# Kernel optimization log

Measured on AMD Instinct MI355X. Metric: run time of the kernel, lower is better.

The kernel has to match this reference:

```python
import jax, jax.numpy as jnp
import numpy as np

N = 100000      # nodes
E = 1600000     # edges (avg degree 16)
D_IN = 256
D_OUT = 128

def setup_inputs() -> dict:
    key = jax.random.key(0)
    k1, k2, k3, k4, k5 = jax.random.split(key, 5)
    x = jax.random.normal(k1, (N, D_IN), dtype=jnp.float32)
    row = jax.random.randint(k2, (E,), 0, N)           # destination node of each edge (adj row index)
    col = jax.random.randint(k3, (E,), 0, N)           # source node (adj col index)
    vals = jnp.ones((E,), dtype=jnp.float32)           # adjacency values
    W = jax.random.normal(k4, (D_IN, D_OUT), dtype=jnp.float32) * (1.0 / np.sqrt(D_IN))
    b = jax.random.normal(k5, (D_OUT,), dtype=jnp.float32) * 0.01
    return {"x": x, "row": row, "col": col, "vals": vals, "W": W, "b": b}

def reference(x, row, col, vals, W, b):
    # support = Linear(x)
    support = x @ W + b                                   # [N, D_OUT]
    # symmetric normalization: D^-1/2 A D^-1/2 (degree = row sums of adj)
    deg = jax.ops.segment_sum(vals, row, num_segments=N)  # [N]
    d_inv_sqrt = jnp.where(deg > 0, jax.lax.rsqrt(jnp.maximum(deg, 1e-12)), 0.0)
    norm_vals = vals * d_inv_sqrt[row] * d_inv_sqrt[col]  # [E]
    # output = spmm(adj_norm, support): gather source features, scale, scatter-add to rows
    out = jax.ops.segment_sum(norm_vals[:, None] * support[col], row, num_segments=N)  # [N, D_OUT]
    return out
```

## Files before the change

kernel.cpp:

```cpp
#include <hip/hip_runtime.h>
#include <hip/hip_bf16.h>

#define DIN 256
#define DOUT 128

typedef float f32x4 __attribute__((ext_vector_type(4)));
typedef __bf16 bf16x8 __attribute__((ext_vector_type(8)));
typedef unsigned short u16x8 __attribute__((ext_vector_type(8)));

__device__ __forceinline__ unsigned short f2bf(float f) {
    __bf16 h = (__bf16)f;
    return *(unsigned short*)&h;
}

__global__ void gcn_wconv(const float* __restrict__ W, unsigned short* __restrict__ Wt) {
    int id = blockIdx.x * blockDim.x + threadIdx.x;
    int c = id >> 8;
    int k = id & 255;
    Wt[c * 256 + k] = f2bf(W[k * DOUT + c]);
}

__global__ __launch_bounds__(256) void gcn_gemm_count(
        const float* __restrict__ x, const unsigned short* __restrict__ Wt,
        const float* __restrict__ bias, unsigned short* __restrict__ support,
        const int* __restrict__ row, int* __restrict__ cnt, int* __restrict__ rank,
        int N, int E, int nbG) {
    __shared__ unsigned short xs[128][72];
    __shared__ unsigned short wl[128][72];

    if ((int)blockIdx.x >= nbG) {
        int e = ((int)blockIdx.x - nbG) * 256 + threadIdx.x;
        if (e < E) rank[e] = atomicAdd(&cnt[row[e]], 1);
        return;
    }

    int t = threadIdx.x;
    int n0 = blockIdx.x * 128;
    int l = t & 63;
    int w = t >> 6;
    int w32 = w * 32;
    int lr = l & 15;
    int lk = (l >> 4) * 8;

    f32x4 acc[2][8] = {};

    int srow = t >> 1;
    int skk = (t & 1) * 32;

    for (int kt = 0; kt < DIN; kt += 64) {
        {
            float4 f[8];
            if (n0 + srow < N) {
                const float4* src = (const float4*)&x[(size_t)(n0 + srow) * DIN + kt + skk];
#pragma unroll
                for (int i = 0; i < 8; ++i) f[i] = src[i];
            } else {
#pragma unroll
                for (int i = 0; i < 8; ++i) f[i] = make_float4(0, 0, 0, 0);
            }
#pragma unroll
            for (int i = 0; i < 4; ++i) {
                u16x8 pk;
                pk[0] = f2bf(f[2 * i].x);     pk[1] = f2bf(f[2 * i].y);
                pk[2] = f2bf(f[2 * i].z);     pk[3] = f2bf(f[2 * i].w);
                pk[4] = f2bf(f[2 * i + 1].x); pk[5] = f2bf(f[2 * i + 1].y);
                pk[6] = f2bf(f[2 * i + 1].z); pk[7] = f2bf(f[2 * i + 1].w);
                *(u16x8*)&xs[srow][skk + 8 * i] = pk;
            }
        }
        {
            const u16x8* src = (const u16x8*)&Wt[(size_t)srow * DIN + kt + skk];
#pragma unroll
            for (int i = 0; i < 4; ++i) *(u16x8*)&wl[srow][skk + 8 * i] = src[i];
        }
        __syncthreads();
#pragma unroll
        for (int ks = 0; ks < 2; ++ks) {
            bf16x8 a[2], b[8];
#pragma unroll
            for (int m = 0; m < 2; ++m)
                a[m] = *(const bf16x8*)&xs[w32 + m * 16 + lr][ks * 32 + lk];
#pragma unroll
            for (int n = 0; n < 8; ++n)
                b[n] = *(const bf16x8*)&wl[n * 16 + lr][ks * 32 + lk];
#pragma unroll
            for (int m = 0; m < 2; ++m)
#pragma unroll
                for (int n = 0; n < 8; ++n)
                    acc[m][n] = __builtin_amdgcn_mfma_f32_16x16x32_bf16(a[m], b[n], acc[m][n], 0, 0, 0);
        }
        __syncthreads();
    }

    float bias_v[8];
#pragma unroll
    for (int n = 0; n < 8; ++n) bias_v[n] = bias[n * 16 + lr];

    int rbase = n0 + w32 + (l >> 4) * 4;
#pragma unroll
    for (int m = 0; m < 2; ++m) {
#pragma unroll
        for (int r = 0; r < 4; ++r) {
            int rowi = rbase + m * 16 + r;
            if (rowi < N) {
                unsigned short* dst = &support[(size_t)rowi * DOUT + lr];
#pragma unroll
                for (int n = 0; n < 8; ++n)
                    dst[n * 16] = f2bf(acc[m][n][r] + bias_v[n]);
            }
        }
    }
}

__global__ void gcn_scan_partial(const int* __restrict__ cnt, int* __restrict__ blk, int N) {
    int b = blockIdx.x, t = threadIdx.x;
    int base = b * 1024 + t * 4;
    int s = 0;
#pragma unroll
    for (int k = 0; k < 4; ++k) { int i = base + k; if (i < N) s += cnt[i]; }
    for (int d = 32; d >= 1; d >>= 1) s += __shfl_down(s, d, 64);
    __shared__ int wsum[4];
    int lane = t & 63, wid = t >> 6;
    if (lane == 0) wsum[wid] = s;
    __syncthreads();
    if (t == 0) blk[b] = wsum[0] + wsum[1] + wsum[2] + wsum[3];
}

__global__ void gcn_scan_blk(int* __restrict__ blk, int nblk) {
    if (threadIdx.x == 0) {
        int run = 0;
        for (int i = 0; i < nblk; ++i) { int v = blk[i]; blk[i] = run; run += v; }
    }
}

__global__ void gcn_scan_final(const int* __restrict__ cnt, const int* __restrict__ blk,
                               int* __restrict__ row_ptr, int N, int E) {
    int b = blockIdx.x, t = threadIdx.x;
    int base = b * 1024 + t * 4;
    int v[4]; int s = 0;
#pragma unroll
    for (int k = 0; k < 4; ++k) { int i = base + k; v[k] = (i < N) ? cnt[i] : 0; s += v[k]; }
    int mysum = s;
    int lane = t & 63, wid = t >> 6;
    for (int d = 1; d < 64; d <<= 1) {
        int tt = __shfl_up(s, d, 64);
        if (lane >= d) s += tt;
    }
    __shared__ int wsum[4];
    if (lane == 63) wsum[wid] = s;
    __syncthreads();
    int woff = 0;
    for (int w = 0; w < wid; ++w) woff += wsum[w];
    int excl = blk[b] + woff + (s - mysum);
#pragma unroll
    for (int k = 0; k < 4; ++k) {
        int i = base + k;
        if (i < N) row_ptr[i] = excl;
        excl += v[k];
    }
    if (b == (int)gridDim.x - 1 && t == (int)blockDim.x - 1) row_ptr[N] = E;
}

__global__ void gcn_fill(const int* __restrict__ row, const int* __restrict__ col,
                         const float* __restrict__ vals, const int* __restrict__ row_ptr,
                         const int* __restrict__ rank, int2* __restrict__ csr, int E) {
    int e = blockIdx.x * blockDim.x + threadIdx.x;
    if (e < E) {
        int r = row[e];
        int p = row_ptr[r] + rank[e];
        int2 pk;
        pk.x = col[e];
        pk.y = __float_as_int(vals[e]);
        csr[p] = pk;
    }
}

__global__ __launch_bounds__(256) void gcn_degdinv(const int* __restrict__ row_ptr,
                                                   const int2* __restrict__ csr,
                                                   float* __restrict__ dinv, int N) {
    int t = threadIdx.x;
    int fl = t & 15;
    int r = blockIdx.x * 16 + (t >> 4);
    if (r >= N) return;
    int beg = row_ptr[r], end = row_ptr[r + 1];
    float s = 0.f;
    for (int j = beg + fl; j < end; j += 16) s += __int_as_float(csr[j].y);
    s += __shfl_xor(s, 1, 64);
    s += __shfl_xor(s, 2, 64);
    s += __shfl_xor(s, 4, 64);
    s += __shfl_xor(s, 8, 64);
    if (fl == 0) dinv[r] = (s > 0.f) ? rsqrtf(fmaxf(s, 1e-12f)) : 0.f;
}

__global__ __launch_bounds__(256) void gcn_norm(const int* __restrict__ row_ptr,
                                                const float* __restrict__ dinv,
                                                int2* __restrict__ csr, int N) {
    int t = threadIdx.x;
    int fl = t & 15;
    int r = blockIdx.x * 16 + (t >> 4);
    if (r >= N) return;
    int beg = row_ptr[r], end = row_ptr[r + 1];
    float dr = dinv[r];
    for (int j = beg + fl; j < end; j += 16) {
        int2 p = csr[j];
        csr[j].y = __float_as_int(__int_as_float(p.y) * dr * dinv[p.x]);
    }
}

__global__ __launch_bounds__(256) void gcn_spmm(const int* __restrict__ row_ptr,
                                                const int2* __restrict__ csr,
                                                const unsigned short* __restrict__ support,
                                                float* __restrict__ out, int N) {
    int wid = threadIdx.x >> 6;
    int lane = threadIdx.x & 63;
    int r = blockIdx.x * 4 + wid;
    if (r >= N) return;
    int beg = row_ptr[r], end = row_ptr[r + 1];
    int g = lane >> 4;
    int fl = lane & 15;
    float acc[8] = {};

    for (int base = beg; base < end; base += 64) {
        int nj = end - base; if (nj > 64) nj = 64;
        int2 e = make_int2(0, 0);
        if (base + lane < end) e = csr[base + lane];
        int nchunk = (nj + 3) >> 2;
        for (int q = 0; q < nchunk; ++q) {
            int idx = q * 4 + g;
            int c = __shfl(e.x, idx, 64);
            float v = __int_as_float(__shfl(e.y, idx, 64));
            if (idx < nj) {
                uint4 p = *(const uint4*)&support[(size_t)c * DOUT + fl * 8];
                acc[0] += v * __uint_as_float(p.x << 16);
                acc[1] += v * __uint_as_float(p.x & 0xffff0000u);
                acc[2] += v * __uint_as_float(p.y << 16);
                acc[3] += v * __uint_as_float(p.y & 0xffff0000u);
                acc[4] += v * __uint_as_float(p.z << 16);
                acc[5] += v * __uint_as_float(p.z & 0xffff0000u);
                acc[6] += v * __uint_as_float(p.w << 16);
                acc[7] += v * __uint_as_float(p.w & 0xffff0000u);
            }
        }
    }
#pragma unroll
    for (int i = 0; i < 8; ++i) {
        acc[i] += __shfl_xor(acc[i], 16, 64);
        acc[i] += __shfl_xor(acc[i], 32, 64);
    }
    if (g == 0) {
        float4 o0, o1;
        o0.x = acc[0]; o0.y = acc[1]; o0.z = acc[2]; o0.w = acc[3];
        o1.x = acc[4]; o1.y = acc[5]; o1.z = acc[6]; o1.w = acc[7];
        float* dst = &out[(size_t)r * DOUT + fl * 8];
        *(float4*)dst = o0;
        *(float4*)(dst + 4) = o1;
    }
}

extern "C" void kernel_launch(void* const* d_in, const int* in_sizes, int n_in,
                              void* d_out, int out_size, void* d_ws, size_t ws_size,
                              hipStream_t stream) {
    const float* x    = (const float*)d_in[0];
    const int*   row  = (const int*)d_in[1];
    const int*   col  = (const int*)d_in[2];
    const float* vals = (const float*)d_in[3];
    const float* W    = (const float*)d_in[4];
    const float* bias = (const float*)d_in[5];
    float* out = (float*)d_out;

    int N = in_sizes[0] / DIN;
    int E = in_sizes[1];
    int NBLK = (N + 1023) / 1024;

    char* ws = (char*)d_ws;
    size_t off = 0;
    auto take = [&](size_t bytes) -> char* {
        char* p = ws + off;
        off = (off + bytes + 255) & ~(size_t)255;
        return p;
    };
    float* dinv    = (float*)take((size_t)N * 4);
    int*   cnt     = (int*)take((size_t)N * 4);
    int*   row_ptr = (int*)take((size_t)(N + 1) * 4);
    int*   blk     = (int*)take((size_t)NBLK * 4);
    int*   rank    = (int*)take((size_t)E * 4);
    int2*  csr     = (int2*)take((size_t)E * 8);
    unsigned short* Wt      = (unsigned short*)take((size_t)DIN * DOUT * 2);
    unsigned short* support = (unsigned short*)take((size_t)N * DOUT * 2);
    (void)ws_size;

    int nbE = (E + 255) / 256;
    int nbG = (N + 127) / 128;

    hipMemsetAsync(cnt, 0, (size_t)N * 4, stream);
    gcn_wconv<<<(DIN * DOUT) / 256, 256, 0, stream>>>(W, Wt);
    gcn_gemm_count<<<nbG + nbE, 256, 0, stream>>>(x, Wt, bias, support, row, cnt, rank, N, E, nbG);
    gcn_scan_partial<<<NBLK, 256, 0, stream>>>(cnt, blk, N);
    gcn_scan_blk<<<1, 64, 0, stream>>>(blk, NBLK);
    gcn_scan_final<<<NBLK, 256, 0, stream>>>(cnt, blk, row_ptr, N, E);
    gcn_fill<<<nbE, 256, 0, stream>>>(row, col, vals, row_ptr, rank, csr, E);
    gcn_degdinv<<<(N + 15) / 16, 256, 0, stream>>>(row_ptr, csr, dinv, N);
    gcn_norm<<<(N + 15) / 16, 256, 0, stream>>>(row_ptr, dinv, csr, N);
    gcn_spmm<<<(N + 3) / 4, 256, 0, stream>>>(row_ptr, csr, support, out, N);
}
```

Before: 390.0 us.

## Fuse edge normalization into SpMM and process two edges per iteration

Removes the separate gcn_norm kernel. The SpMM now multiplies each edge value by dinv[col] at gather time and scales the accumulated row by dinv[row] at the end. This drops one kernel launch and a full read-modify-write pass over the CSR array, at the cost of an extra dinv gather per edge inside SpMM. The inner loop is also unrolled to issue two independent support loads per iteration, which should raise memory-level parallelism.

```diff
diff --git a/kernel.cpp b/kernel.cpp
--- a/kernel.cpp
+++ b/kernel.cpp
@@ -192,23 +192,9 @@
     if (fl == 0) dinv[r] = (s > 0.f) ? rsqrtf(fmaxf(s, 1e-12f)) : 0.f;
 }
 
-__global__ __launch_bounds__(256) void gcn_norm(const int* __restrict__ row_ptr,
-                                                const float* __restrict__ dinv,
-                                                int2* __restrict__ csr, int N) {
-    int t = threadIdx.x;
-    int fl = t & 15;
-    int r = blockIdx.x * 16 + (t >> 4);
-    if (r >= N) return;
-    int beg = row_ptr[r], end = row_ptr[r + 1];
-    float dr = dinv[r];
-    for (int j = beg + fl; j < end; j += 16) {
-        int2 p = csr[j];
-        csr[j].y = __float_as_int(__int_as_float(p.y) * dr * dinv[p.x]);
-    }
-}
-
 __global__ __launch_bounds__(256) void gcn_spmm(const int* __restrict__ row_ptr,
                                                 const int2* __restrict__ csr,
+                                                const float* __restrict__ dinv,
                                                 const unsigned short* __restrict__ support,
                                                 float* __restrict__ out, int N) {
     int wid = threadIdx.x >> 6;
@@ -224,22 +210,36 @@
         int nj = end - base; if (nj > 64) nj = 64;
         int2 e = make_int2(0, 0);
         if (base + lane < end) e = csr[base + lane];
-        int nchunk = (nj + 3) >> 2;
+        int nchunk = (nj + 7) >> 3;
         for (int q = 0; q < nchunk; ++q) {
-            int idx = q * 4 + g;
-            int c = __shfl(e.x, idx, 64);
-            float v = __int_as_float(__shfl(e.y, idx, 64));
-            if (idx < nj) {
-                uint4 p = *(const uint4*)&support[(size_t)c * DOUT + fl * 8];
-                acc[0] += v * __uint_as_float(p.x << 16);
-                acc[1] += v * __uint_as_float(p.x & 0xffff0000u);
-                acc[2] += v * __uint_as_float(p.y << 16);
-                acc[3] += v * __uint_as_float(p.y & 0xffff0000u);
-                acc[4] += v * __uint_as_float(p.z << 16);
-                acc[5] += v * __uint_as_float(p.z & 0xffff0000u);
-                acc[6] += v * __uint_as_float(p.w << 16);
-                acc[7] += v * __uint_as_float(p.w & 0xffff0000u);
-            }
+            int ia = q * 8 + g;
+            int ib = ia + 4;
+            int ca = __shfl(e.x, ia, 64);
+            float va = __int_as_float(__shfl(e.y, ia, 64));
+            int cb = __shfl(e.x, ib, 64);
+            float vb = __int_as_float(__shfl(e.y, ib, 64));
+            bool pa = ia < nj, pb = ib < nj;
+            uint4 sa = make_uint4(0, 0, 0, 0), sb = make_uint4(0, 0, 0, 0);
+            float da = 0.f, db = 0.f;
+            if (pa) { da = dinv[ca]; sa = *(const uint4*)&support[(size_t)ca * DOUT + fl * 8]; }
+            if (pb) { db = dinv[cb]; sb = *(const uint4*)&support[(size_t)cb * DOUT + fl * 8]; }
+            va *= da; vb *= db;
+            acc[0] += va * __uint_as_float(sa.x << 16);
+            acc[1] += va * __uint_as_float(sa.x & 0xffff0000u);
+            acc[2] += va * __uint_as_float(sa.y << 16);
+            acc[3] += va * __uint_as_float(sa.y & 0xffff0000u);
+            acc[4] += va * __uint_as_float(sa.z << 16);
+            acc[5] += va * __uint_as_float(sa.z & 0xffff0000u);
+            acc[6] += va * __uint_as_float(sa.w << 16);
+            acc[7] += va * __uint_as_float(sa.w & 0xffff0000u);
+            acc[0] += vb * __uint_as_float(sb.x << 16);
+            acc[1] += vb * __uint_as_float(sb.x & 0xffff0000u);
+            acc[2] += vb * __uint_as_float(sb.y << 16);
+            acc[3] += vb * __uint_as_float(sb.y & 0xffff0000u);
+            acc[4] += vb * __uint_as_float(sb.z << 16);
+            acc[5] += vb * __uint_as_float(sb.z & 0xffff0000u);
+            acc[6] += vb * __uint_as_float(sb.w << 16);
+            acc[7] += vb * __uint_as_float(sb.w & 0xffff0000u);
         }
     }
 #pragma unroll
@@ -248,9 +248,10 @@
         acc[i] += __shfl_xor(acc[i], 32, 64);
     }
     if (g == 0) {
+        float dr = dinv[r];
         float4 o0, o1;
-        o0.x = acc[0]; o0.y = acc[1]; o0.z = acc[2]; o0.w = acc[3];
-        o1.x = acc[4]; o1.y = acc[5]; o1.z = acc[6]; o1.w = acc[7];
+        o0.x = acc[0] * dr; o0.y = acc[1] * dr; o0.z = acc[2] * dr; o0.w = acc[3] * dr;
+        o1.x = acc[4] * dr; o1.y = acc[5] * dr; o1.z = acc[6] * dr; o1.w = acc[7] * dr;
         float* dst = &out[(size_t)r * DOUT + fl * 8];
         *(float4*)dst = o0;
         *(float4*)(dst + 4) = o1;
@@ -300,6 +301,5 @@
     gcn_scan_final<<<NBLK, 256, 0, stream>>>(cnt, blk, row_ptr, N, E);
     gcn_fill<<<nbE, 256, 0, stream>>>(row, col, vals, row_ptr, rank, csr, E);
     gcn_degdinv<<<(N + 15) / 16, 256, 0, stream>>>(row_ptr, csr, dinv, N);
-    gcn_norm<<<(N + 15) / 16, 256, 0, stream>>>(row_ptr, dinv, csr, N);
-    gcn_spmm<<<(N + 3) / 4, 256, 0, stream>>>(row_ptr, csr, support, out, N);
-}
+    gcn_spmm<<<(N + 3) / 4, 256, 0, stream>>>(row_ptr, csr, dinv, support, out, N);
+}
```

Result: faster. 376.7 us (-3.4%).
